# Optimization experiments

Hardware: AMD Instinct MI355X
Metric: run time of the kernel (lower is better)

Reference implementation:

```python
import jax, jax.numpy as jnp
import numpy as np

EPS = 0.01


def setup_inputs() -> dict:
    key = jax.random.key(0)
    ks = jax.random.split(key, 7)
    B, N, H = 4, 1024, 64
    pos = jax.random.normal(ks[0], (B, N, 3), dtype=jnp.float32)
    # MLP params (Linear stores weight as [out,in]; we keep [in,out] for x @ W)
    W1 = jax.random.normal(ks[1], (1, H), dtype=jnp.float32) * (1.0 / np.sqrt(1))
    b1 = jax.random.normal(ks[2], (H,), dtype=jnp.float32) * 0.01
    W2 = jax.random.normal(ks[3], (H, H), dtype=jnp.float32) * (1.0 / np.sqrt(H))
    b2 = jax.random.normal(ks[4], (H,), dtype=jnp.float32) * 0.01
    W3 = jax.random.normal(ks[5], (H, 1), dtype=jnp.float32) * (1.0 / np.sqrt(H))
    b3 = jax.random.normal(ks[6], (1,), dtype=jnp.float32) * 0.01
    return {"pos": pos, "W1": W1, "b1": b1, "W2": W2, "b2": b2, "W3": W3, "b3": b3}


def reference(pos, W1, b1, W2, b2, W3, b3):
    B, N, _ = pos.shape
    # pairwise soft distances, only upper-triangular pairs (i < j)
    idx_i, idx_j = jnp.triu_indices(N, k=1)                      # [P], P = N(N-1)/2
    diff = pos[:, idx_i, :] - pos[:, idx_j, :]                   # [B, P, 3]
    dist_soft = jnp.sqrt(jnp.sum(diff * diff, axis=-1) + EPS * EPS)  # [B, P]
    d = dist_soft[..., None]                                     # [B, P, 1]
    h = jax.nn.silu(d @ W1 + b1)                                 # [B, P, H]
    h = jax.nn.silu(h @ W2 + b2)                                 # [B, P, H]
    u = (h @ W3 + b3)[..., 0]                                    # [B, P]
    U = jnp.sum(u, axis=1, keepdims=True) / N                    # [B, 1]
    return U
```

## Files before the change

kernel.cpp:

```cpp
#include <hip/hip_runtime.h>


constexpr int N_ATOMS = 1024;
constexpr int H = 64;
constexpr int NB = 4;
constexpr float EPS = 0.01f;

constexpr int NT = 1024;
constexpr int NNODES = NT + 1;
constexpr float TMAX = 16.0f;
constexpr float INV_H = (float)NT / TMAX;
constexpr double DH = (double)TMAX / (double)NT;

constexpr int BLOCK = 256;
constexpr int ITILES = N_ATOMS / 64;
constexpr int JCHUNKS = 8;
constexpr int NBLK = NB * ITILES * JCHUNKS;
constexpr int JPW = 32;

__device__ __forceinline__ float4 make_coef(float2 n0, float2 n1) {
    float dp = n1.x - n0.x;
    float c2 = fmaf(3.0f, dp, -fmaf(2.0f, n0.y, n1.y));
    float c3 = fmaf(-2.0f, dp, n0.y + n1.y);
    return make_float4(n0.x, n0.y, c2, c3);
}
__device__ __forceinline__ float heval(float4 c, float fr) {
    return fmaf(fr, fmaf(fr, fmaf(fr, c.w, c.z), c.y), c.x);
}

__global__ __launch_bounds__(64) void build_table(
    const float* __restrict__ W1, const float* __restrict__ b1,
    const float* __restrict__ W2, const float* __restrict__ b2,
    const float* __restrict__ W3, const float* __restrict__ b3,
    float2* __restrict__ nodes)
{
    const int node = blockIdx.x;
    const int lane = threadIdx.x;
    const double d = (double)node * DH;

    double a1 = d * (double)W1[lane] + (double)b1[lane];
    double s1 = 1.0 / (1.0 + exp(-a1));
    double h1 = a1 * s1;
    double g1 = (s1 + a1 * s1 * (1.0 - s1)) * (double)W1[lane];

    double acc = (double)b2[lane], dacc = 0.0;
    for (int k = 0; k < H; ++k) {
        double hk = __shfl(h1, k);
        double gk = __shfl(g1, k);
        double w  = (double)W2[k * H + lane];
        acc  += hk * w;
        dacc += gk * w;
    }
    double s2  = 1.0 / (1.0 + exp(-acc));
    double h2  = acc * s2;
    double dh2 = (s2 + acc * s2 * (1.0 - s2)) * dacc;

    double pu = h2  * (double)W3[lane];
    double du = dh2 * (double)W3[lane];
    for (int off = 32; off; off >>= 1) {
        pu += __shfl_down(pu, off);
        du += __shfl_down(du, off);
    }
    if (lane == 0)
        nodes[node] = make_float2((float)((double)b3[0] + pu), (float)(du * DH));
}

__global__ __launch_bounds__(BLOCK) void hnn_pair(
    const float* __restrict__ pos, const float2* __restrict__ nodes,
    double* __restrict__ partials)
{
    __shared__ float4 posl4[N_ATOMS * 3 / 4];
    __shared__ float4 coef[NT];
    __shared__ float wred[BLOCK / 64];

    const int bid  = blockIdx.x;
    const int b    = bid >> 7;
    const int r    = bid & 127;
    const int ibase = (r >> 3) * 64;
    const int jbase = (r & 7) * 128;
    const int tid  = (int)threadIdx.x;

    const float4* p4 = (const float4*)(pos + (size_t)b * N_ATOMS * 3);
#pragma unroll
    for (int rr = 0; rr < 3; ++rr)
        posl4[tid + BLOCK * rr] = p4[tid + BLOCK * rr];
#pragma unroll
    for (int rr = 0; rr < NT / BLOCK; ++rr) {
        int k = tid + BLOCK * rr;
        coef[k] = make_coef(nodes[k], nodes[k + 1]);
    }
    __syncthreads();

    const float* posf = (const float*)posl4;
    const int lane = tid & 63;
    const int w    = tid >> 6;
    const int i    = ibase + lane;
    const float xi = posf[3 * i], yi = posf[3 * i + 1], zi = posf[3 * i + 2];

    float acc = 0.0f;
    const int j0 = jbase + w * JPW;
#pragma unroll
    for (int s = 0; s < JPW; ++s) {
        const int j = j0 + s;
        float dx = xi - posf[3 * j];
        float dy = yi - posf[3 * j + 1];
        float dz = zi - posf[3 * j + 2];
        float d  = sqrtf(fmaf(dx, dx, fmaf(dy, dy, fmaf(dz, dz, EPS * EPS))));
        float t  = d * INV_H;
        int   k  = min((int)t, NT - 1);
        float fr = t - (float)k;
        acc += heval(coef[k], fr);
    }

    for (int off = 32; off; off >>= 1) acc += __shfl_down(acc, off);
    if (lane == 0) wred[w] = acc;
    __syncthreads();
    if (tid == 0)
        partials[bid] = (double)((wred[0] + wred[1]) + (wred[2] + wred[3]));
}

__global__ __launch_bounds__(BLOCK) void hnn_finalize(
    const float2* __restrict__ nodes, const double* __restrict__ partials,
    float* __restrict__ out)
{
    const int tid  = (int)threadIdx.x;
    const int b    = tid >> 6;
    const int lane = tid & 63;
    double s = partials[b * 128 + lane] + partials[b * 128 + 64 + lane];
    for (int off = 32; off; off >>= 1) s += __shfl_down(s, off);
    if (lane == 0) {
        float d  = sqrtf(fmaf(0.0f, 0.0f, fmaf(0.0f, 0.0f,
                         fmaf(0.0f, 0.0f, EPS * EPS))));
        float t  = d * INV_H;
        int   k  = min((int)t, NT - 1);
        float fr = t - (float)k;
        float fe = heval(make_coef(nodes[k], nodes[k + 1]), fr);
        out[b] = (float)((s - (double)N_ATOMS * (double)fe)
                         * (0.5 / (double)N_ATOMS));
    }
}

extern "C" void kernel_launch(void* const* d_in, const int* in_sizes, int n_in,
                              void* d_out, int out_size, void* d_ws, size_t ws_size,
                              hipStream_t stream) {
    const float* pos = (const float*)d_in[0];
    const float* W1  = (const float*)d_in[1];
    const float* b1  = (const float*)d_in[2];
    const float* W2  = (const float*)d_in[3];
    const float* b2  = (const float*)d_in[4];
    const float* W3  = (const float*)d_in[5];
    const float* b3  = (const float*)d_in[6];

    float2* nodes    = (float2*)d_ws;
    double* partials = (double*)((char*)d_ws + 16384);
    float*  out      = (float*)d_out;

    hipLaunchKernelGGL(build_table, dim3(NNODES), dim3(64), 0, stream,
                       W1, b1, W2, b2, W3, b3, nodes);
    hipLaunchKernelGGL(hnn_pair, dim3(NBLK), dim3(BLOCK), 0, stream,
                       pos, nodes, partials);
    hipLaunchKernelGGL(hnn_finalize, dim3(1), dim3(BLOCK), 0, stream,
                       nodes, partials, out);
}
```

Measured before the change: 79.01 us.

## Fuse finalize into pair kernel via last-block atomic counter; pack table warps

Removes the separate finalize kernel launch by having each pair block increment an atomic counter after writing its partial. The last block to arrive reduces all partials and writes the output. The table builder now packs four node-wavefronts per 256-thread block instead of one 64-thread block per node, and it resets the counter. This cuts one launch and its gap, but adds a threadfence and an atomic per block.

```diff
diff --git a/kernel.cpp b/kernel.cpp
--- a/kernel.cpp
+++ b/kernel.cpp
@@ -13,9 +13,7 @@
 constexpr double DH = (double)TMAX / (double)NT;
 
 constexpr int BLOCK = 256;
-constexpr int ITILES = N_ATOMS / 64;
-constexpr int JCHUNKS = 8;
-constexpr int NBLK = NB * ITILES * JCHUNKS;
+constexpr int NBLK = 512;
 constexpr int JPW = 32;
 
 __device__ __forceinline__ float4 make_coef(float2 n0, float2 n1) {
@@ -28,15 +26,21 @@
     return fmaf(fr, fmaf(fr, fmaf(fr, c.w, c.z), c.y), c.x);
 }
 
-__global__ __launch_bounds__(64) void build_table(
+__global__ __launch_bounds__(BLOCK) void build_table(
     const float* __restrict__ W1, const float* __restrict__ b1,
     const float* __restrict__ W2, const float* __restrict__ b2,
     const float* __restrict__ W3, const float* __restrict__ b3,
-    float2* __restrict__ nodes)
+    float2* __restrict__ nodes, unsigned* __restrict__ done)
 {
-    const int node = blockIdx.x;
-    const int lane = threadIdx.x;
-    const double d = (double)node * DH;
+    const int tid  = (int)threadIdx.x;
+    const int lane = tid & 63;
+    const int w    = tid >> 6;
+    const int gw   = (int)blockIdx.x * (BLOCK / 64) + w;
+
+    if (blockIdx.x == 0 && tid == 0) *done = 0u;
+
+    if (gw >= NNODES) return;
+    const double d = (double)gw * DH;
 
     double a1 = d * (double)W1[lane] + (double)b1[lane];
     double s1 = 1.0 / (1.0 + exp(-a1));
@@ -47,9 +51,9 @@
     for (int k = 0; k < H; ++k) {
         double hk = __shfl(h1, k);
         double gk = __shfl(g1, k);
-        double w  = (double)W2[k * H + lane];
-        acc  += hk * w;
-        dacc += gk * w;
+        double wt = (double)W2[k * H + lane];
+        acc  += hk * wt;
+        dacc += gk * wt;
     }
     double s2  = 1.0 / (1.0 + exp(-acc));
     double h2  = acc * s2;
@@ -62,23 +66,27 @@
         du += __shfl_down(du, off);
     }
     if (lane == 0)
-        nodes[node] = make_float2((float)((double)b3[0] + pu), (float)(du * DH));
+        nodes[gw] = make_float2((float)((double)b3[0] + pu), (float)(du * DH));
 }
 
-__global__ __launch_bounds__(BLOCK) void hnn_pair(
+__global__ __launch_bounds__(BLOCK) void pair_fin(
     const float* __restrict__ pos, const float2* __restrict__ nodes,
-    double* __restrict__ partials)
+    double* __restrict__ partials, unsigned* __restrict__ done,
+    float* __restrict__ out)
 {
     __shared__ float4 posl4[N_ATOMS * 3 / 4];
     __shared__ float4 coef[NT];
     __shared__ float wred[BLOCK / 64];
+    __shared__ bool  amLast;
 
-    const int bid  = blockIdx.x;
-    const int b    = bid >> 7;
-    const int r    = bid & 127;
+    const int tid   = (int)threadIdx.x;
+    const int bid   = (int)blockIdx.x;
+    const int lane  = tid & 63;
+    const int w     = tid >> 6;
+    const int b     = bid >> 7;
+    const int r     = bid & 127;
     const int ibase = (r >> 3) * 64;
     const int jbase = (r & 7) * 128;
-    const int tid  = (int)threadIdx.x;
 
     const float4* p4 = (const float4*)(pos + (size_t)b * N_ATOMS * 3);
 #pragma unroll
@@ -92,9 +100,7 @@
     __syncthreads();
 
     const float* posf = (const float*)posl4;
-    const int lane = tid & 63;
-    const int w    = tid >> 6;
-    const int i    = ibase + lane;
+    const int i = ibase + lane;
     const float xi = posf[3 * i], yi = posf[3 * i + 1], zi = posf[3 * i + 2];
 
     float acc = 0.0f;
@@ -115,28 +121,30 @@
     for (int off = 32; off; off >>= 1) acc += __shfl_down(acc, off);
     if (lane == 0) wred[w] = acc;
     __syncthreads();
-    if (tid == 0)
+
+    if (tid == 0) {
         partials[bid] = (double)((wred[0] + wred[1]) + (wred[2] + wred[3]));
-}
+        __threadfence();
+        unsigned prev = atomicAdd(done, 1u);
+        amLast = (prev == (unsigned)(NBLK - 1));
+    }
+    __syncthreads();
 
-__global__ __launch_bounds__(BLOCK) void hnn_finalize(
-    const float2* __restrict__ nodes, const double* __restrict__ partials,
-    float* __restrict__ out)
-{
-    const int tid  = (int)threadIdx.x;
-    const int b    = tid >> 6;
-    const int lane = tid & 63;
-    double s = partials[b * 128 + lane] + partials[b * 128 + 64 + lane];
-    for (int off = 32; off; off >>= 1) s += __shfl_down(s, off);
-    if (lane == 0) {
-        float d  = sqrtf(fmaf(0.0f, 0.0f, fmaf(0.0f, 0.0f,
-                         fmaf(0.0f, 0.0f, EPS * EPS))));
-        float t  = d * INV_H;
-        int   k  = min((int)t, NT - 1);
-        float fr = t - (float)k;
-        float fe = heval(make_coef(nodes[k], nodes[k + 1]), fr);
-        out[b] = (float)((s - (double)N_ATOMS * (double)fe)
-                         * (0.5 / (double)N_ATOMS));
+    if (amLast) {
+        __threadfence();
+        const volatile double* vp = (const volatile double*)partials;
+        double s = vp[w * 128 + lane] + vp[w * 128 + 64 + lane];
+        for (int off = 32; off; off >>= 1) s += __shfl_down(s, off);
+        if (lane == 0) {
+            float dd = sqrtf(fmaf(0.0f, 0.0f, fmaf(0.0f, 0.0f,
+                             fmaf(0.0f, 0.0f, EPS * EPS))));
+            float t  = dd * INV_H;
+            int   k  = min((int)t, NT - 1);
+            float fr = t - (float)k;
+            float fe = heval(make_coef(nodes[k], nodes[k + 1]), fr);
+            out[w] = (float)((s - (double)N_ATOMS * (double)fe)
+                             * (0.5 / (double)N_ATOMS));
+        }
     }
 }
 
@@ -151,14 +159,13 @@
     const float* W3  = (const float*)d_in[5];
     const float* b3  = (const float*)d_in[6];
 
-    float2* nodes    = (float2*)d_ws;
-    double* partials = (double*)((char*)d_ws + 16384);
-    float*  out      = (float*)d_out;
+    float2*   nodes    = (float2*)d_ws;
+    double*   partials = (double*)((char*)d_ws + 16384);
+    unsigned* done     = (unsigned*)((char*)d_ws + 20480);
+    float*    out      = (float*)d_out;
 
-    hipLaunchKernelGGL(build_table, dim3(NNODES), dim3(64), 0, stream,
-                       W1, b1, W2, b2, W3, b3, nodes);
-    hipLaunchKernelGGL(hnn_pair, dim3(NBLK), dim3(BLOCK), 0, stream,
-                       pos, nodes, partials);
-    hipLaunchKernelGGL(hnn_finalize, dim3(1), dim3(BLOCK), 0, stream,
-                       nodes, partials, out);
+    hipLaunchKernelGGL(build_table, dim3((NNODES + 3) / 4), dim3(BLOCK), 0,
+                       stream, W1, b1, W2, b2, W3, b3, nodes, done);
+    hipLaunchKernelGGL(pair_fin, dim3(NBLK), dim3(BLOCK), 0, stream,
+                       pos, nodes, partials, done, out);
 }
```

Result: slower. 87.20 us (+10.4%).
